# Kernel optimization log

Measured on AMD Instinct MI355X. Metric: run time of the kernel, lower is better.

The kernel has to match this reference:

```python
import jax, jax.numpy as jnp
import numpy as np

NUM_HEADS = 16
ROPE_BASE = 10000.0


def _rope_tables(head_dim, seq_len, dtype=jnp.float32):
    # Half-split convention: rotate first half against second half.
    inv_freq = 1.0 / (ROPE_BASE ** (jnp.arange(0, head_dim, 2, dtype=dtype) / head_dim))
    pos = jnp.arange(seq_len, dtype=dtype)
    angles_half = jnp.einsum('s,d->sd', pos, inv_freq)          # (S, D/2)
    angles = jnp.concatenate([angles_half, angles_half], -1)     # (S, D)
    return jnp.cos(angles), jnp.sin(angles)


def _apply_rope(x, cos, sin):
    # x: (H, S, D); cos/sin: (S, D) broadcast over heads
    half = x.shape[-1] // 2
    x1, x2 = x[..., :half], x[..., half:]
    x_rot = jnp.concatenate([-x2, x1], axis=-1)
    return x * cos + x_rot * sin


def setup_inputs() -> dict:
    key = jax.random.key(0)
    S, E = 2048, 2048
    ks = jax.random.split(key, 9)
    sc = 0.02
    return {
        'x': jax.random.normal(ks[0], (S, E), jnp.float32),
        'Wq': jax.random.normal(ks[1], (E, E), jnp.float32) * sc,
        'bq': jax.random.normal(ks[2], (E,), jnp.float32) * sc,
        'Wk': jax.random.normal(ks[3], (E, E), jnp.float32) * sc,
        'bk': jax.random.normal(ks[4], (E,), jnp.float32) * sc,
        'Wv': jax.random.normal(ks[5], (E, E), jnp.float32) * sc,
        'bv': jax.random.normal(ks[6], (E,), jnp.float32) * sc,
        'Wo': jax.random.normal(ks[7], (E, E), jnp.float32) * sc,
        'bo': jax.random.normal(ks[8], (E,), jnp.float32) * sc,
    }


def reference(x, Wq, bq, Wk, bk, Wv, bv, Wo, bo):
    S, E = x.shape
    H = NUM_HEADS
    D = E // H
    scale = D ** 0.5
    cos, sin = _rope_tables(D, S, x.dtype)

    def proj(W, b):
        return (x @ W.T + b).reshape(S, H, D).transpose(1, 0, 2)  # (H, S, D)

    q = _apply_rope(proj(Wq, bq), cos, sin)
    k = _apply_rope(proj(Wk, bk), cos, sin)
    v = proj(Wv, bv)

    scores = jnp.einsum('hsd,htd->hst', q, k) / scale  # (H, S, S)
    attn = jax.nn.softmax(scores, axis=-1)
    out = jnp.einsum('hst,htd->hsd', attn, v)          # (H, S, D)
    # Faithful to the original's transpose(0,1).view(S,E) on a (1,H,S,D)
    # tensor: an in-order (head-major) flatten reinterpreted as (S, E).
    out = out.reshape(S, E)
    return out @ Wo.T + bo
```

## Files before the change

### kernel.cpp

```cpp
#include <hip/hip_runtime.h>

#define SDIM 2048
#define EDIM 2048
#define NHEAD 16
#define DHEAD 128

typedef __attribute__((ext_vector_type(8))) short short8;
typedef __attribute__((ext_vector_type(4))) float floatx4;

__device__ __forceinline__ float bf2f(ushort u) {
    union { uint i; float f; } v; v.i = ((uint)u) << 16; return v.f;
}
__device__ __forceinline__ ushort f2bf(float f) {
    union { float f; uint i; } v; v.f = f;
    uint r = v.i + 0x7fff + ((v.i >> 16) & 1);
    return (ushort)(r >> 16);
}

__device__ __forceinline__ void gload_lds16(const ushort* g, ushort* l) {
    __builtin_amdgcn_global_load_lds(
        (const __attribute__((address_space(1))) void*)g,
        (__attribute__((address_space(3))) void*)l, 16, 0, 0);
}

__global__ void convert4_kernel(
    const float* __restrict__ s0, const float* __restrict__ s1,
    const float* __restrict__ s2, const float* __restrict__ s3,
    ushort* __restrict__ d0, ushort* __restrict__ d1,
    ushort* __restrict__ d2, ushort* __restrict__ d3)
{
    const float* src; ushort* dst;
    switch (blockIdx.y) {
        case 0: src = s0; dst = d0; break;
        case 1: src = s1; dst = d1; break;
        case 2: src = s2; dst = d2; break;
        default: src = s3; dst = d3; break;
    }
    int i = blockIdx.x * blockDim.x + threadIdx.x;
    float4 f = ((const float4*)src)[i];
    ushort4 o;
    o.x = f2bf(f.x); o.y = f2bf(f.y); o.z = f2bf(f.z); o.w = f2bf(f.w);
    ((ushort4*)dst)[i] = o;
}

#define QPRESCALE 0.12754245f

__global__ __launch_bounds__(512, 2) void gemm256_qkv(
    const ushort* __restrict__ A,
    const ushort* __restrict__ B0, const ushort* __restrict__ B1, const ushort* __restrict__ B2,
    const float* __restrict__ s0, const float* __restrict__ s1, const float* __restrict__ s2,
    ushort* __restrict__ C0, ushort* __restrict__ C1, ushort* __restrict__ Vtg,
    const float* __restrict__ WoF, ushort* __restrict__ WoB)
{
    __shared__ __align__(16) ushort smem[2][2][2][128 * 64];

    const int tid  = threadIdx.x;

    if (blockIdx.y >= 24) {
        const int idx = (blockIdx.y - 24) * 8 + blockIdx.x;
        const float4* src = (const float4*)WoF;
#pragma unroll
        for (int it = 0; it < 32; ++it) {
            int i = idx * 16384 + it * 512 + tid;
            float4 f = src[i];
            ushort4 o;
            o.x = f2bf(f.x); o.y = f2bf(f.y); o.z = f2bf(f.z); o.w = f2bf(f.w);
            ((ushort4*)WoB)[i] = o;
        }
        return;
    }

    const int lane = tid & 63;
    const int wave = tid >> 6;
    const int l15 = lane & 15, quad = lane >> 4, l7 = lane & 7;
    const int wm = wave & 1, wn = wave >> 1;
    const int bm = blockIdx.x * 256;
    const int which = blockIdx.y >> 3;
    const int n0 = (blockIdx.y & 7) * 256;
    const int NT = EDIM / 64;

    const ushort* Bsel = (which == 0) ? B0 : (which == 1) ? B1 : B2;
    const float*  bia  = (which == 0) ? s0 : (which == 1) ? s1 : s2;

    const int srow = tid >> 3;
    const int sgc  = (((tid & 7) ^ ((tid >> 3) & 7)) << 3);

    floatx4 acc[8][4];
#pragma unroll
    for (int i = 0; i < 8; i++)
#pragma unroll
        for (int j = 0; j < 4; j++) acc[i][j] = (floatx4)0.0f;

    auto stageA = [&](int tile, int h) {
        const ushort* g = A + (size_t)(bm + h * 128 + srow) * EDIM + tile * 64 + sgc;
        ushort* l = &smem[tile & 1][0][h][0] + tid * 8;
        gload_lds16(g, l);
        gload_lds16(g + (size_t)64 * EDIM, l + 4096);
    };
    auto stageB = [&](int tile, int h) {
        const ushort* g = Bsel + (size_t)(n0 + h * 128 + srow) * EDIM + tile * 64 + sgc;
        ushort* l = &smem[tile & 1][1][h][0] + tid * 8;
        gload_lds16(g, l);
        gload_lds16(g + (size_t)64 * EDIM, l + 4096);
    };

    stageA(0, 0); stageA(0, 1); stageB(0, 0); stageB(0, 1);
    stageB(1, 0); stageB(1, 1);
    asm volatile("s_waitcnt vmcnt(4)" ::: "memory");
    __builtin_amdgcn_s_barrier();

    const int c0 = ((quad ^ l7) << 3);
    const int c1 = (((quad + 4) ^ l7) << 3);
    const int brow0 = (wn & 1) * 64;

    short8 af[4], b0[4], b1[4];

#define MFMA16(AOFF, AF, BF) \
    _Pragma("unroll") \
    for (int mf = 0; mf < 4; mf++) \
        _Pragma("unroll") \
        for (int an = 0; an < 4; an++) \
            acc[(AOFF) + mf][an] = __builtin_amdgcn_mfma_f32_16x16x32_bf16( \
                AF[mf], BF[an], acc[(AOFF) + mf][an], 0, 0, 0);

#define PH_PRE() do { \
    asm volatile("" ::: "memory"); \
    __builtin_amdgcn_s_barrier(); \
    asm volatile("s_waitcnt lgkmcnt(0)" ::: "memory"); \
    __builtin_amdgcn_sched_barrier(0); \
    __builtin_amdgcn_s_setprio(1); \
} while (0)
#define PH_POST() do { \
    __builtin_amdgcn_s_setprio(0); \
    asm volatile("" ::: "memory"); \
    __builtin_amdgcn_s_barrier(); \
} while (0)

    for (int t = 0; t < NT; ++t) {
        const ushort* aH = &smem[t & 1][0][wm][0];
        const ushort* bH = &smem[t & 1][1][wn >> 1][0];

#pragma unroll
        for (int mf = 0; mf < 4; mf++)
            af[mf] = *(const short8*)(aH + (mf * 16 + l15) * 64 + c0);
#pragma unroll
        for (int an = 0; an < 4; an++)
            b0[an] = *(const short8*)(bH + (brow0 + an * 16 + l15) * 64 + c0);
        if (t + 1 < NT) stageA(t + 1, 0);
        PH_PRE();
        MFMA16(0, af, b0);
        PH_POST();

        short8 ag[4];
#pragma unroll
        for (int mf = 0; mf < 4; mf++)
            ag[mf] = *(const short8*)(aH + (mf * 16 + l15) * 64 + c1);
#pragma unroll
        for (int an = 0; an < 4; an++)
            b1[an] = *(const short8*)(bH + (brow0 + an * 16 + l15) * 64 + c1);
        if (t + 1 < NT) stageA(t + 1, 1);
        PH_PRE();
        MFMA16(0, ag, b1);
        PH_POST();

#pragma unroll
        for (int mf = 0; mf < 4; mf++)
            af[mf] = *(const short8*)(aH + (64 + mf * 16 + l15) * 64 + c0);
        if (t + 2 < NT) stageB(t + 2, 0);
        PH_PRE();
        MFMA16(4, af, b0);
        PH_POST();

#pragma unroll
        for (int mf = 0; mf < 4; mf++)
            ag[mf] = *(const short8*)(aH + (64 + mf * 16 + l15) * 64 + c1);
        if (t + 2 < NT) stageB(t + 2, 1);
        asm volatile("" ::: "memory");
        __builtin_amdgcn_s_barrier();
        asm volatile("s_waitcnt lgkmcnt(0)" ::: "memory");
        __builtin_amdgcn_sched_barrier(0);
        __builtin_amdgcn_s_setprio(1);
        MFMA16(4, ag, b1);
        __builtin_amdgcn_s_setprio(0);
        if (t < NT - 2) asm volatile("s_waitcnt vmcnt(4)" ::: "memory");
        else            asm volatile("s_waitcnt vmcnt(0)" ::: "memory");
        __builtin_amdgcn_s_barrier();
    }
#undef MFMA16
#undef PH_PRE
#undef PH_POST

    if (which == 2) {
#pragma unroll
        for (int an = 0; an < 4; an++) {
            int col = n0 + wn * 64 + an * 16 + l15;
            int h = col >> 7, d = col & 127;
            float bv = bia[col];
            ushort* cp = Vtg + (size_t)h * SDIM * DHEAD + (size_t)d * SDIM;
#pragma unroll
            for (int am = 0; am < 8; am++) {
                int s = bm + wm * 128 + am * 16 + quad * 4;
                ushort4 pk;
                pk.x = f2bf(acc[am][an][0] + bv);
                pk.y = f2bf(acc[am][an][1] + bv);
                pk.z = f2bf(acc[am][an][2] + bv);
                pk.w = f2bf(acc[am][an][3] + bv);
                *(ushort4*)(cp + s) = pk;
            }
        }
    } else {
        ushort* C = (which == 0) ? C0 : C1;
        const float psc = (which == 0) ? QPRESCALE : 1.0f;
        float* xch = (float*)smem;
        float bv[4], invf[4];
#pragma unroll
        for (int an = 0; an < 4; an++) {
            bv[an]   = bia[n0 + wn * 64 + an * 16 + l15];
            invf[an] = __expf((float)(an * 16 + l15) * -0.14391157f);
        }
        const int mybase = wave * 1024 + quad * 16 + l15;
        const int pbase  = (wave ^ 2) * 1024 + quad * 16 + l15;
        const int rowb = bm + wm * 128 + quad * 4;
#pragma unroll
        for (int am2 = 0; am2 < 4; am2++) {
            __syncthreads();
#pragma unroll
            for (int sl = 0; sl < 2; sl++) {
                int am = am2 * 2 + sl;
#pragma unroll
                for (int an = 0; an < 4; an++)
#pragma unroll
                    for (int r = 0; r < 4; r++)
                        xch[sl * 8192 + mybase + an * 256 + r * 64] = acc[am][an][r] + bv[an];
            }
            __syncthreads();
#pragma unroll
            for (int sl = 0; sl < 2; sl++) {
                int am = am2 * 2 + sl;
#pragma unroll
                for (int an = 0; an < 4; an++) {
                    int col = n0 + wn * 64 + an * 16 + l15;
#pragma unroll
                    for (int r = 0; r < 4; r++) {
                        int row = rowb + am * 16 + r;
                        float v = acc[am][an][r] + bv[an];
                        float w = xch[sl * 8192 + pbase + an * 256 + r * 64];
                        float ang = (float)row * invf[an];
                        float rev = ang * 0.15915494309f;
                        rev -= floorf(rev);
                        float arad = rev * 6.28318530718f;
                        float sn = __sinf(arad), cs = __cosf(arad);
                        float o = ((wn & 1) == 0) ? (v * cs - w * sn) : (v * cs + w * sn);
                        C[(size_t)row * EDIM + col] = f2bf(o * psc);
                    }
                }
            }
        }
    }
}

template <typename OUTT, int KSPLIT>
__global__ __launch_bounds__(256) void gemm_bt(
    const ushort* __restrict__ A,
    const ushort* __restrict__ B0, const ushort* __restrict__ B1, const ushort* __restrict__ B2,
    const float* __restrict__ s0, const float* __restrict__ s1, const float* __restrict__ s2,
    OUTT* __restrict__ C0, OUTT* __restrict__ C1, OUTT* __restrict__ C2,
    int nbpm)
{
    __shared__ __align__(16) ushort smem[2 * 128 * 32];
    ushort* a_s = smem;
    ushort* b_s = smem + 128 * 32;

    const int tid = threadIdx.x;
    const int wave = tid >> 6, lane = tid & 63;
    const int l15 = lane & 15, quad = lane >> 4;
    const int wm = wave & 1, wn = wave >> 1;
    const int bm = blockIdx.x * 128;
    const int which = blockIdx.y / nbpm;
    const int n0 = (blockIdx.y % nbpm) * 128;

    const ushort* B;
    const float*  bia;
    OUTT*         C;
    const ushort* Abase;
    if constexpr (KSPLIT == 2) {
        B = B0; bia = s0; C = C0;
        Abase = A + which * (EDIM / 2);
    } else {
        B   = (which == 0) ? B0 : (which == 1) ? B1 : B2;
        bia = (which == 0) ? s0 : (which == 1) ? s1 : s2;
        C   = (which == 0) ? C0 : (which == 1) ? C1 : C2;
        Abase = A;
    }
    const ushort* Bbase = (KSPLIT == 2) ? B + which * (EDIM / 2) : B;

    floatx4 acc[4][4];
#pragma unroll
    for (int i = 0; i < 4; i++)
#pragma unroll
        for (int j = 0; j < 4; j++) acc[i][j] = (floatx4)0.0f;

    const int t1 = tid + 256;
    const int row0 = tid >> 2, kc0 = (tid & 3) * 8;
    const int row1 = t1 >> 2,  kc1 = (t1 & 3) * 8;

    for (int k0 = 0; k0 < EDIM / KSPLIT; k0 += 32) {
        __syncthreads();
        gload_lds16(Abase + (size_t)(bm + row0) * EDIM + k0 + kc0, a_s + tid * 8);
        gload_lds16(Abase + (size_t)(bm + row1) * EDIM + k0 + kc1, a_s + t1 * 8);
        gload_lds16(Bbase + (size_t)(n0 + row0) * EDIM + k0 + kc0, b_s + tid * 8);
        gload_lds16(Bbase + (size_t)(n0 + row1) * EDIM + k0 + kc1, b_s + t1 * 8);
        __syncthreads();

        short8 af[4], bf[4];
#pragma unroll
        for (int mt = 0; mt < 4; mt++)
            af[mt] = *(const short8*)(a_s + (wm * 64 + mt * 16 + l15) * 32 + quad * 8);
#pragma unroll
        for (int nt = 0; nt < 4; nt++)
            bf[nt] = *(const short8*)(b_s + (wn * 64 + nt * 16 + l15) * 32 + quad * 8);
#pragma unroll
        for (int mt = 0; mt < 4; mt++)
#pragma unroll
            for (int nt = 0; nt < 4; nt++)
                acc[mt][nt] = __builtin_amdgcn_mfma_f32_16x16x32_bf16(af[mt], bf[nt], acc[mt][nt], 0, 0, 0);
    }

    if constexpr (KSPLIT == 2) {
#pragma unroll
        for (int nt = 0; nt < 4; nt++) {
            int col = n0 + wn * 64 + nt * 16 + l15;
            float bv = (which == 0) ? bia[col] : 0.0f;
#pragma unroll
            for (int mt = 0; mt < 4; mt++) {
#pragma unroll
                for (int r = 0; r < 4; r++) {
                    int row = bm + wm * 64 + mt * 16 + quad * 4 + r;
                    atomicAdd(&((float*)C)[(size_t)row * EDIM + col], acc[mt][nt][r] + bv);
                }
            }
        }
    } else {
#pragma unroll
        for (int nt = 0; nt < 4; nt++) {
            int col = n0 + wn * 64 + nt * 16 + l15;
            float bv = bia[col];
#pragma unroll
            for (int mt = 0; mt < 4; mt++) {
#pragma unroll
                for (int r = 0; r < 4; r++) {
                    int row = bm + wm * 64 + mt * 16 + quad * 4 + r;
                    float v = acc[mt][nt][r] + bv;
                    if constexpr (sizeof(OUTT) == 2)
                        ((ushort*)C)[(size_t)row * EDIM + col] = f2bf(v);
                    else
                        ((float*)C)[(size_t)row * EDIM + col] = v;
                }
            }
        }
    }
}

#define MFIX2 17.31234049f
__global__ __launch_bounds__(256, 4) void attn_kernel(
    const ushort* __restrict__ Q, const ushort* __restrict__ K,
    const ushort* __restrict__ Vtg,
    ushort* __restrict__ Opart, float* __restrict__ Lsum,
    ushort* __restrict__ Ab, int nsplit)
{
    __shared__ __align__(16) ushort Ks[64 * 128];
    __shared__ __align__(16) ushort Vt[128 * 64];
    __shared__ __align__(16) ushort Ps[64 * 64];

    const int bid = blockIdx.x;
    const int head = bid & 15, qt = (bid >> 4) & 31, half = bid >> 9;
    const int tid = threadIdx.x, wave = tid >> 6, lane = tid & 63;
    const int l15 = lane & 15, quad = lane >> 4;
    const int l7 = l15 & 7;
    const int kstart = half * (SDIM / nsplit);
    const int ntile = (SDIM / nsplit) / 64;

    short8 qf[4];
    {
        int s = qt * 64 + wave * 16 + l15;
        const ushort* qp = Q + (size_t)s * EDIM + head * DHEAD;
#pragma unroll
        for (int kc = 0; kc < 4; kc++) qf[kc] = *(const short8*)(qp + kc * 32 + quad * 8);
    }

    floatx4 o[8];
#pragma unroll
    for (int i = 0; i < 8; i++) o[i] = (floatx4)0.0f;
    float lsum = 0.0f;

    const int krow = tid >> 4, kc8 = tid & 15;
    const int vd = tid >> 3, vc8 = tid & 7;
    const int prow = wave * 16 + l15;

    for (int kv = 0; kv < ntile; kv++) {
        const int k0 = kstart + kv * 64;
        __syncthreads();
#pragma unroll
        for (int i = 0; i < 4; i++) {
            int row = krow + i * 16;
            uint4 v = *(const uint4*)(K + (size_t)(k0 + row) * EDIM + head * DHEAD + kc8 * 8);
            *(uint4*)(Ks + row * 128 + ((kc8 ^ (row & 7)) << 3)) = v;
        }
#pragma unroll
        for (int i = 0; i < 4; i++) {
            int d = vd + i * 32;
            uint4 v = *(const uint4*)(Vtg + (size_t)head * SDIM * DHEAD + (size_t)d * SDIM + k0 + vc8 * 8);
            *(uint4*)(Vt + d * 64 + ((vc8 ^ (d & 7)) << 3)) = v;
        }
        __syncthreads();

#pragma unroll
        for (int nt = 0; nt < 4; nt++) {
            floatx4 st = (floatx4)0.0f;
            __builtin_amdgcn_s_setprio(1);
#pragma unroll
            for (int kc = 0; kc < 4; kc++) {
                short8 kfr = *(const short8*)(Ks + (nt * 16 + l15) * 128 + (((kc * 4 + quad) ^ l7) << 3));
                st = __builtin_amdgcn_mfma_f32_16x16x32_bf16(kfr, qf[kc], st, 0, 0, 0);
            }
            __builtin_amdgcn_s_setprio(0);
            ushort4 pk;
            float p0 = __builtin_amdgcn_exp2f(st[0] - MFIX2);
            float p1 = __builtin_amdgcn_exp2f(st[1] - MFIX2);
            float p2 = __builtin_amdgcn_exp2f(st[2] - MFIX2);
            float p3 = __builtin_amdgcn_exp2f(st[3] - MFIX2);
            lsum += (p0 + p1) + (p2 + p3);
            pk.x = f2bf(p0); pk.y = f2bf(p1); pk.z = f2bf(p2); pk.w = f2bf(p3);
            int c2 = (nt * 2 + (quad >> 1)) ^ l7;
            *(ushort4*)(Ps + prow * 64 + (c2 << 3) + ((quad & 1) << 2)) = pk;
        }

        __builtin_amdgcn_s_setprio(1);
#pragma unroll
        for (int kc2 = 0; kc2 < 2; kc2++) {
            short8 af = *(const short8*)(Ps + prow * 64 + (((kc2 * 4 + quad) ^ l7) << 3));
#pragma unroll
            for (int nt2 = 0; nt2 < 8; nt2++) {
                short8 bfr = *(const short8*)(Vt + (nt2 * 16 + l15) * 64 + (((kc2 * 4 + quad) ^ l7) << 3));
                o[nt2] = __builtin_amdgcn_mfma_f32_16x16x32_bf16(af, bfr, o[nt2], 0, 0, 0);
            }
        }
        __builtin_amdgcn_s_setprio(0);
    }

    lsum += __shfl_xor(lsum, 16);
    lsum += __shfl_xor(lsum, 32);

    if (nsplit == 1) {
        float invl[4];
#pragma unroll
        for (int r = 0; r < 4; r++) invl[r] = 1.0f / __shfl(lsum, quad * 4 + r, 16);
#pragma unroll
        for (int nt2 = 0; nt2 < 8; nt2++) {
#pragma unroll
            for (int r = 0; r < 4; r++) {
                int s = qt * 64 + wave * 16 + quad * 4 + r;
                int d = nt2 * 16 + l15;
                Ab[(size_t)head * SDIM * DHEAD + (size_t)s * DHEAD + d] = f2bf(o[nt2][r] * invl[r]);
            }
        }
    } else {
        size_t pb = ((size_t)half * NHEAD + head) * SDIM * DHEAD;
#pragma unroll
        for (int nt2 = 0; nt2 < 8; nt2++) {
#pragma unroll
            for (int r = 0; r < 4; r++) {
                int s = qt * 64 + wave * 16 + quad * 4 + r;
                int d = nt2 * 16 + l15;
                Opart[pb + (size_t)s * DHEAD + d] = f2bf(o[nt2][r]);
            }
        }
        if (lane < 16)
            Lsum[((size_t)half * NHEAD + head) * SDIM + qt * 64 + wave * 16 + lane] = lsum;
    }
}

__global__ void merge_kernel(const ushort* __restrict__ Opart,
                             const float* __restrict__ Lsum,
                             ushort* __restrict__ Ab)
{
    const int HS = NHEAD * SDIM;
    int t = blockIdx.x * blockDim.x + threadIdx.x;
    int row = t >> 4, c8 = (t & 15) * 8;
    float inv = 1.0f / (Lsum[row] + Lsum[HS + row]);
    float acc[8] = {0, 0, 0, 0, 0, 0, 0, 0};
#pragma unroll
    for (int p = 0; p < 2; p++) {
        union { uint4 v; ushort u[8]; } a;
        a.v = *(const uint4*)(Opart + (size_t)p * HS * DHEAD + (size_t)row * DHEAD + c8);
#pragma unroll
        for (int j = 0; j < 8; j++) acc[j] += bf2f(a.u[j]);
    }
    union { uint4 v; ushort u[8]; } ro;
#pragma unroll
    for (int j = 0; j < 8; j++) ro.u[j] = f2bf(acc[j] * inv);
    *(uint4*)(Ab + (size_t)row * DHEAD + c8) = ro.v;
}

extern "C" void kernel_launch(void* const* d_in, const int* in_sizes, int n_in,
                              void* d_out, int out_size, void* d_ws, size_t ws_size,
                              hipStream_t stream) {
    (void)in_sizes; (void)n_in; (void)out_size;
    const float* x  = (const float*)d_in[0];
    const float* Wq = (const float*)d_in[1];
    const float* bq = (const float*)d_in[2];
    const float* Wk = (const float*)d_in[3];
    const float* bk = (const float*)d_in[4];
    const float* Wv = (const float*)d_in[5];
    const float* bv = (const float*)d_in[6];
    const float* Wo = (const float*)d_in[7];
    const float* bo = (const float*)d_in[8];
    float* out = (float*)d_out;

    char* ws = (char*)d_ws;
    const size_t SEG = (size_t)EDIM * EDIM * 2;
    ushort* xb  = (ushort*)(ws + 0 * SEG);
    ushort* Wqb = (ushort*)(ws + 1 * SEG);
    ushort* Wkb = (ushort*)(ws + 2 * SEG);
    ushort* Wvb = (ushort*)(ws + 3 * SEG);
    ushort* Wob = (ushort*)(ws + 4 * SEG);
    ushort* Qb  = (ushort*)(ws + 5 * SEG);
    ushort* Kb  = (ushort*)(ws + 6 * SEG);
    ushort* Vtg = (ushort*)(ws + 7 * SEG);
    ushort* Ab  = (ushort*)(ws + 8 * SEG);
    ushort* Op  = (ushort*)(ws + 0 * SEG);
    float*  Ls  = (float*)(ws + 11 * SEG);

    const int split = (ws_size >= ((size_t)89 << 20)) ? 1 : 0;

    convert4_kernel<<<dim3(4096, 4), 256, 0, stream>>>(
        x, Wq, Wk, Wv, xb, Wqb, Wkb, Wvb);

    gemm256_qkv<<<dim3(8, 32), 512, 0, stream>>>(
        xb, Wqb, Wkb, Wvb, bq, bk, bv, Qb, Kb, Vtg, Wo, Wob);

    if (split) {
        attn_kernel<<<1024, 256, 0, stream>>>(Qb, Kb, Vtg, Op, Ls, Ab, 2);
        merge_kernel<<<2048, 256, 0, stream>>>(Op, Ls, Ab);
        hipMemsetAsync(out, 0, (size_t)EDIM * EDIM * 4, stream);
        gemm_bt<float, 2><<<dim3(16, 32), 256, 0, stream>>>(
            Ab, Wob, Wob, Wob, bo, bo, bo, out, out, out, 16);
    } else {
        attn_kernel<<<512, 256, 0, stream>>>(Qb, Kb, Vtg, Op, Ls, Ab, 1);
        gemm_bt<float, 1><<<dim3(16, 16), 256, 0, stream>>>(
            Ab, Wob, Wob, Wob, bo, bo, bo, out, out, out, 16);
    }
}
```

Measured before the change: 293.7 us.

## Fuse split-K attention merge into attention kernel via per-tile arrival counters

The separate merge kernel is replaced by an in-kernel reduction. Each attention block writes its partial output and row sum, bumps an atomic counter for its (head, query-tile), and the second arriving block reads the other half's partial through LDS, combines and normalizes it, and writes the final bf16 output. The output memset is also folded into the attention blocks, which zero the fp32 output buffer before the split-K output GEMM accumulates into it. This removes two launches and one pass over the partials, at the cost of atomics, a threadfence, an extra LDS round trip, and counters that the convert kernel must reset on every call.

Measured after the change: 430.9 us. 46.7% more time.

```diff
diff --git a/kernel.cpp b/kernel.cpp
--- a/kernel.cpp
+++ b/kernel.cpp
@@ -27,8 +27,13 @@
     const float* __restrict__ s0, const float* __restrict__ s1,
     const float* __restrict__ s2, const float* __restrict__ s3,
     ushort* __restrict__ d0, ushort* __restrict__ d1,
-    ushort* __restrict__ d2, ushort* __restrict__ d3)
+    ushort* __restrict__ d2, ushort* __restrict__ d3,
+    uint* __restrict__ cnt)
 {
+    if (blockIdx.x == 0 && blockIdx.y == 0) {
+        cnt[threadIdx.x] = 0;
+        cnt[threadIdx.x + 256] = 0;
+    }
     const float* src; ushort* dst;
     switch (blockIdx.y) {
         case 0: src = s0; dst = d0; break;
@@ -366,11 +371,13 @@
     const ushort* __restrict__ Q, const ushort* __restrict__ K,
     const ushort* __restrict__ Vtg,
     ushort* __restrict__ Opart, float* __restrict__ Lsum,
-    ushort* __restrict__ Ab, int nsplit)
+    ushort* __restrict__ Ab, int nsplit,
+    uint* __restrict__ cnt, float* __restrict__ outz)
 {
     __shared__ __align__(16) ushort Ks[64 * 128];
     __shared__ __align__(16) ushort Vt[128 * 64];
     __shared__ __align__(16) ushort Ps[64 * 64];
+    __shared__ uint sOld;
 
     const int bid = blockIdx.x;
     const int head = bid & 15, qt = (bid >> 4) & 31, half = bid >> 9;
@@ -379,6 +386,13 @@
     const int l7 = l15 & 7;
     const int kstart = half * (SDIM / nsplit);
     const int ntile = (SDIM / nsplit) / 64;
+
+    if (nsplit != 1) {
+        float4* oz = (float4*)outz;
+#pragma unroll
+        for (int z = 0; z < 4; ++z)
+            oz[(size_t)bid * 1024 + z * 256 + tid] = (float4){0.f, 0.f, 0.f, 0.f};
+    }
 
     short8 qf[4];
     {
@@ -477,29 +491,39 @@
         }
         if (lane < 16)
             Lsum[((size_t)half * NHEAD + head) * SDIM + qt * 64 + wave * 16 + lane] = lsum;
-    }
-}
-
-__global__ void merge_kernel(const ushort* __restrict__ Opart,
-                             const float* __restrict__ Lsum,
-                             ushort* __restrict__ Ab)
-{
-    const int HS = NHEAD * SDIM;
-    int t = blockIdx.x * blockDim.x + threadIdx.x;
-    int row = t >> 4, c8 = (t & 15) * 8;
-    float inv = 1.0f / (Lsum[row] + Lsum[HS + row]);
-    float acc[8] = {0, 0, 0, 0, 0, 0, 0, 0};
-#pragma unroll
-    for (int p = 0; p < 2; p++) {
-        union { uint4 v; ushort u[8]; } a;
-        a.v = *(const uint4*)(Opart + (size_t)p * HS * DHEAD + (size_t)row * DHEAD + c8);
-#pragma unroll
-        for (int j = 0; j < 8; j++) acc[j] += bf2f(a.u[j]);
-    }
-    union { uint4 v; ushort u[8]; } ro;
-#pragma unroll
-    for (int j = 0; j < 8; j++) ro.u[j] = f2bf(acc[j] * inv);
-    *(uint4*)(Ab + (size_t)row * DHEAD + c8) = ro.v;
+
+        __threadfence();
+        __syncthreads();
+        if (tid == 0) sOld = atomicAdd(&cnt[head * 32 + qt], 1u);
+        __syncthreads();
+        if (sOld == 1) {
+            const int oh = half ^ 1;
+            const uint4* gs = (const uint4*)(Opart +
+                ((size_t)(oh * NHEAD + head)) * SDIM * DHEAD + (size_t)(qt * 64) * DHEAD);
+            uint4* kd = (uint4*)Ks;
+            kd[tid]       = gs[tid];
+            kd[tid + 256] = gs[tid + 256];
+            kd[tid + 512] = gs[tid + 512];
+            kd[tid + 768] = gs[tid + 768];
+            float l2 = Lsum[((size_t)oh * NHEAD + head) * SDIM + qt * 64 + wave * 16 + l15];
+            float tot = lsum + l2;
+            __syncthreads();
+            float invl[4];
+#pragma unroll
+            for (int r = 0; r < 4; r++) invl[r] = 1.0f / __shfl(tot, quad * 4 + r, 16);
+#pragma unroll
+            for (int nt2 = 0; nt2 < 8; nt2++) {
+#pragma unroll
+                for (int r = 0; r < 4; r++) {
+                    int sl = wave * 16 + quad * 4 + r;
+                    int d = nt2 * 16 + l15;
+                    float v = o[nt2][r] + bf2f(Ks[sl * 128 + d]);
+                    Ab[(size_t)head * SDIM * DHEAD + (size_t)(qt * 64 + sl) * DHEAD + d] =
+                        f2bf(v * invl[r]);
+                }
+            }
+        }
+    }
 }
 
 extern "C" void kernel_launch(void* const* d_in, const int* in_sizes, int n_in,
@@ -530,23 +554,22 @@
     ushort* Ab  = (ushort*)(ws + 8 * SEG);
     ushort* Op  = (ushort*)(ws + 0 * SEG);
     float*  Ls  = (float*)(ws + 11 * SEG);
+    uint*   Cnt = (uint*)(ws + 11 * SEG + (512 << 10));
 
     const int split = (ws_size >= ((size_t)89 << 20)) ? 1 : 0;
 
     convert4_kernel<<<dim3(4096, 4), 256, 0, stream>>>(
-        x, Wq, Wk, Wv, xb, Wqb, Wkb, Wvb);
+        x, Wq, Wk, Wv, xb, Wqb, Wkb, Wvb, Cnt);
 
     gemm256_qkv<<<dim3(8, 32), 512, 0, stream>>>(
         xb, Wqb, Wkb, Wvb, bq, bk, bv, Qb, Kb, Vtg, Wo, Wob);
 
     if (split) {
-        attn_kernel<<<1024, 256, 0, stream>>>(Qb, Kb, Vtg, Op, Ls, Ab, 2);
-        merge_kernel<<<2048, 256, 0, stream>>>(Op, Ls, Ab);
-        hipMemsetAsync(out, 0, (size_t)EDIM * EDIM * 4, stream);
+        attn_kernel<<<1024, 256, 0, stream>>>(Qb, Kb, Vtg, Op, Ls, Ab, 2, Cnt, out);
         gemm_bt<float, 2><<<dim3(16, 32), 256, 0, stream>>>(
             Ab, Wob, Wob, Wob, bo, bo, bo, out, out, out, 16);
     } else {
-        attn_kernel<<<512, 256, 0, stream>>>(Qb, Kb, Vtg, Op, Ls, Ab, 1);
+        attn_kernel<<<512, 256, 0, stream>>>(Qb, Kb, Vtg, Op, Ls, Ab, 1, Cnt, out);
         gemm_bt<float, 1><<<dim3(16, 16), 256, 0, stream>>>(
             Ab, Wob, Wob, Wob, bo, bo, bo, out, out, out, 16);
     }
```
